# Performance work log

Hardware: AMD Instinct MI355X
Metric: run time of the kernel (lower is better)

The kernel has to match this reference:

```python
import jax, jax.numpy as jnp
import numpy as np

B, N, TOKEN_DIM = 8, 1024, 768
H, D = 12, 64  # n_heads, head_dim


def setup_inputs() -> dict:
    key = jax.random.key(0)
    k1, k2, k3, k4 = jax.random.split(key, 4)
    x = jax.random.normal(k1, (B, N, TOKEN_DIM), dtype=jnp.float32)
    # nn.Linear(token_dim, 3*H*D, bias=False); store as (in, out)
    W_qkv = jax.random.normal(k2, (TOKEN_DIM, 3 * H * D), dtype=jnp.float32) * (TOKEN_DIM ** -0.5)
    # nn.Linear(H*D, token_dim) with bias
    W_out = jax.random.normal(k3, (H * D, TOKEN_DIM), dtype=jnp.float32) * ((H * D) ** -0.5)
    b_out = jax.random.normal(k4, (TOKEN_DIM,), dtype=jnp.float32) * 0.01
    return {"x": x, "W_qkv": W_qkv, "W_out": W_out, "b_out": b_out}


def reference(x, W_qkv, W_out, b_out):
    b, n, _ = x.shape
    qkv = x @ W_qkv                              # (B, N, 3*H*D)
    # Faithful to original: reshape directly to (B, 3, H, N, D)
    qkv = qkv.reshape(b, 3, H, n, D)
    q, k, v = qkv[:, 0], qkv[:, 1], qkv[:, 2]    # each (B, H, N, D)
    scale = D ** -0.5
    scores = jnp.einsum('bhnd,bhmd->bhnm', q, k) * scale
    probs = jax.nn.softmax(scores, axis=-1)
    attn = jnp.einsum('bhnm,bhmd->bhnd', probs, v)  # (B, H, N, D)
    attn = attn.transpose(0, 2, 1, 3).reshape(b, n, H * D)
    out = attn @ W_out + b_out                    # dropout p=0.0 is identity
    return out
```

## Files before the change

kernel.cpp:

```cpp
#include <hip/hip_runtime.h>
#include <math.h>

static constexpr int NB   = 8;
static constexpr int SEQ  = 1024;
static constexpr int TD   = 768;
static constexpr int NH   = 12;
static constexpr int HD   = 64;
static constexpr int QKVC = 3 * NH * HD;

static constexpr size_t BATCH_ELEMS = (size_t)SEQ * QKVC;
static constexpr size_t THIRD_ELEMS = (size_t)NH * SEQ * HD;
static constexpr size_t HEAD_ELEMS  = (size_t)SEQ * HD;

typedef __bf16 bf16x8 __attribute__((ext_vector_type(8)));
typedef __bf16 bf16x4 __attribute__((ext_vector_type(4)));
typedef float  f32x4  __attribute__((ext_vector_type(4)));

#define MFMA16(a, b, c) __builtin_amdgcn_mfma_f32_16x16x32_bf16((a), (b), (c), 0, 0, 0)

static constexpr float SCL2E = 0.18033688011112042f;

__device__ __forceinline__ void gload_lds16(const void* g, void* l) {
  __builtin_amdgcn_global_load_lds(
      (const __attribute__((address_space(1))) unsigned int*)g,
      (__attribute__((address_space(3))) unsigned int*)l, 16, 0, 0);
}

__global__ __launch_bounds__(256) void cast_f32_bf16(const float* __restrict__ in,
                                                     __bf16* __restrict__ out, int n4) {
  int i = blockIdx.x * 256 + threadIdx.x;
  if (i < n4) {
    float4 v = ((const float4*)in)[i];
    bf16x4 o;
    o[0] = (__bf16)v.x; o[1] = (__bf16)v.y; o[2] = (__bf16)v.z; o[3] = (__bf16)v.w;
    ((bf16x4*)out)[i] = o;
  }
}

__global__ __launch_bounds__(256) void wtrans(const float* __restrict__ W,
                                              __bf16* __restrict__ Wt, int K, int N) {
  __shared__ float T[32 * 33];
  const int tid = threadIdx.x;
  const int k0 = blockIdx.y * 32, n0 = blockIdx.x * 32;
#pragma unroll
  for (int i = 0; i < 4; ++i) {
    int idx = tid + i * 256;
    int kk = idx >> 5, nn = idx & 31;
    T[kk * 33 + nn] = W[(size_t)(k0 + kk) * N + n0 + nn];
  }
  __syncthreads();
#pragma unroll
  for (int i = 0; i < 4; ++i) {
    int idx = tid + i * 256;
    int nn = idx >> 5, kk = idx & 31;
    Wt[(size_t)(n0 + nn) * K + k0 + kk] = (__bf16)T[kk * 33 + nn];
  }
}

__global__ __launch_bounds__(256) void vtrans(const __bf16* __restrict__ qkvb,
                                              __bf16* __restrict__ vtb) {
  const int nt = blockIdx.x;
  const int h = blockIdx.y;
  const int b = blockIdx.z;
  __shared__ __bf16 T[128 * 72];
  const int tid = threadIdx.x;
  const int n0 = nt * 128;
  const __bf16* Vb = qkvb + (size_t)b * BATCH_ELEMS + 2 * THIRD_ELEMS + (size_t)h * HEAD_ELEMS;
#pragma unroll
  for (int i = 0; i < 4; ++i) {
    int ch = tid + i * 256;
    int row = ch >> 3, c8 = ch & 7;
    *(bf16x8*)&T[row * 72 + c8 * 8] = *(const bf16x8*)&Vb[(size_t)(n0 + row) * HD + c8 * 8];
  }
  __syncthreads();
#pragma unroll
  for (int i = 0; i < 4; ++i) {
    int ch = tid + i * 256;
    int d = ch >> 4, n8 = ch & 15;
    bf16x8 v;
#pragma unroll
    for (int j = 0; j < 8; ++j) v[j] = T[(n8 * 8 + j) * 72 + d];
    *(bf16x8*)&vtb[((size_t)((b * NH + h) * HD) + d) * SEQ + n0 + n8 * 8] = v;
  }
}

template <int OUT_BF16>
__global__ __launch_bounds__(256) void gemm_mfma(const __bf16* __restrict__ A,
                                                 const __bf16* __restrict__ Bt,
                                                 const float* __restrict__ bias,
                                                 void* __restrict__ C,
                                                 int M, int N, int K) {
  __shared__ __bf16 As[128 * 32];
  __shared__ __bf16 Bs[128 * 32];
  const int tid = threadIdx.x;
  const int lane = tid & 63;
  const int wid = tid >> 6;
  const int wr = wid >> 1, wc = wid & 1;
  const int r = lane & 15, g = lane >> 4;
  const size_t bm = (size_t)blockIdx.y * 128;
  const size_t bn = (size_t)blockIdx.x * 128;

  const int srow = lane >> 2;
  const int scol = (lane & 3) * 8;

  f32x4 acc[4][4];
#pragma unroll
  for (int mi = 0; mi < 4; ++mi)
#pragma unroll
    for (int nj = 0; nj < 4; ++nj) acc[mi][nj] = (f32x4){0.f, 0.f, 0.f, 0.f};

  for (int k0 = 0; k0 < K; k0 += 32) {
#pragma unroll
    for (int j = 0; j < 2; ++j) {
      const int rowbase = wid * 32 + j * 16;
      gload_lds16(&A[(bm + rowbase + srow) * K + k0 + scol], &As[rowbase * 32]);
      gload_lds16(&Bt[(bn + rowbase + srow) * K + k0 + scol], &Bs[rowbase * 32]);
    }
    __syncthreads();
    bf16x8 af[4], bf[4];
#pragma unroll
    for (int mi = 0; mi < 4; ++mi)
      af[mi] = *(const bf16x8*)&As[(wr * 64 + mi * 16 + r) * 32 + g * 8];
#pragma unroll
    for (int nj = 0; nj < 4; ++nj)
      bf[nj] = *(const bf16x8*)&Bs[(wc * 64 + nj * 16 + r) * 32 + g * 8];
#pragma unroll
    for (int mi = 0; mi < 4; ++mi)
#pragma unroll
      for (int nj = 0; nj < 4; ++nj)
        acc[mi][nj] = MFMA16(af[mi], bf[nj], acc[mi][nj]);
    __syncthreads();
  }

  const int orow0 = g * 4;
  const int ocol = r;
#pragma unroll
  for (int mi = 0; mi < 4; ++mi)
#pragma unroll
    for (int nj = 0; nj < 4; ++nj)
#pragma unroll
      for (int reg = 0; reg < 4; ++reg) {
        size_t rrow = bm + wr * 64 + mi * 16 + orow0 + reg;
        size_t ccol = bn + wc * 64 + nj * 16 + ocol;
        float v = acc[mi][nj][reg];
        if (OUT_BF16)
          ((__bf16*)C)[rrow * N + ccol] = (__bf16)v;
        else
          ((float*)C)[rrow * N + ccol] = v + bias[ccol];
      }
}

__global__ __launch_bounds__(256) void attn_mfma(const __bf16* __restrict__ qkvb,
                                                 const __bf16* __restrict__ vtb,
                                                 __bf16* __restrict__ attn2b) {
  const int d = blockIdx.x;
  const int qt = (d >> 3) & 7;
  const int hb = (d >> 6) * 8 + (d & 7);
  const int b = hb / NH, h = hb % NH;

  const int tid = threadIdx.x;
  const int lane = tid & 63;
  const int w = tid >> 6;
  const int c = lane & 15, g = lane >> 4;

  __shared__ __bf16 KsF[2][4096];
  __shared__ __bf16 VsF[2][4096];

  const __bf16* Qb = qkvb + (size_t)b * BATCH_ELEMS + (size_t)h * HEAD_ELEMS;
  const __bf16* Kb = Qb + THIRD_ELEMS;
  const __bf16* Vtb = vtb + (size_t)((b * NH + h) * HD) * SEQ;

  const __bf16* kS[2];
  const __bf16* vS[2];
  int ldsOff[2];
#pragma unroll
  for (int i = 0; i < 2; ++i) {
    const int t2f = i * 4 + w;
    const int t = t2f >> 1, f = t2f & 1;
    const int krow = ((t >> 1) << 5) | ((c >> 2) << 3) | ((t & 1) << 2) | (c & 3);
    kS[i] = Kb + krow * HD + f * 32 + g * 8;
    const int db = t2f >> 1, kk = t2f & 1;
    vS[i] = Vtb + (db * 16 + c) * SEQ + kk * 32 + g * 8;
    ldsOff[i] = t2f * 512;
  }

  bf16x8 qf[2][2];
#pragma unroll
  for (int s = 0; s < 2; ++s) {
    const int q0s = qt * 128 + s * 64 + w * 16;
#pragma unroll
    for (int f = 0; f < 2; ++f)
      qf[s][f] = *(const bf16x8*)&Qb[(size_t)(q0s + c) * HD + f * 32 + g * 8];
  }

  f32x4 Oa[2][4];
#pragma unroll
  for (int s = 0; s < 2; ++s)
#pragma unroll
    for (int db = 0; db < 4; ++db) Oa[s][db] = (f32x4){0.f, 0.f, 0.f, 0.f};
  float lpart[2] = {0.f, 0.f};

#pragma unroll
  for (int i = 0; i < 2; ++i) {
    gload_lds16(kS[i], &KsF[0][ldsOff[i]]);
    gload_lds16(vS[i], &VsF[0][ldsOff[i]]);
    kS[i] += 64 * HD;
    vS[i] += 64;
  }
  __syncthreads();

  int cur = 0;
  for (int it = 0; it < SEQ / 64; ++it) {
    if (it < SEQ / 64 - 1) {
      const int nxt = cur ^ 1;
#pragma unroll
      for (int i = 0; i < 2; ++i) {
        gload_lds16(kS[i], &KsF[nxt][ldsOff[i]]);
        gload_lds16(vS[i], &VsF[nxt][ldsOff[i]]);
        kS[i] += 64 * HD;
        vS[i] += 64;
      }
    }

    f32x4 sa[2][4];
#pragma unroll
    for (int s = 0; s < 2; ++s)
#pragma unroll
      for (int t = 0; t < 4; ++t) sa[s][t] = (f32x4){0.f, 0.f, 0.f, 0.f};
#pragma unroll
    for (int t = 0; t < 4; ++t)
#pragma unroll
      for (int f = 0; f < 2; ++f) {
        bf16x8 kf = *(const bf16x8*)&KsF[cur][(t * 2 + f) * 512 + lane * 8];
        sa[0][t] = MFMA16(kf, qf[0][f], sa[0][t]);
        sa[1][t] = MFMA16(kf, qf[1][f], sa[1][t]);
      }

    bf16x8 pb[2][2];
#pragma unroll
    for (int s = 0; s < 2; ++s) {
      float p[4][4];
      float lp = 0.f;
#pragma unroll
      for (int t = 0; t < 4; ++t)
#pragma unroll
        for (int reg = 0; reg < 4; ++reg) {
          float pv = __builtin_exp2f(sa[s][t][reg] * SCL2E);
          p[t][reg] = pv;
          lp += pv;
        }
      lpart[s] += lp;
#pragma unroll
      for (int kk = 0; kk < 2; ++kk)
#pragma unroll
        for (int i = 0; i < 4; ++i) {
          pb[s][kk][i] = (__bf16)p[2 * kk][i];
          pb[s][kk][4 + i] = (__bf16)p[2 * kk + 1][i];
        }
    }

#pragma unroll
    for (int db = 0; db < 4; ++db)
#pragma unroll
      for (int kk = 0; kk < 2; ++kk) {
        bf16x8 vf = *(const bf16x8*)&VsF[cur][(db * 2 + kk) * 512 + lane * 8];
        Oa[0][db] = MFMA16(vf, pb[0][kk], Oa[0][db]);
        Oa[1][db] = MFMA16(vf, pb[1][kk], Oa[1][db]);
      }

    __syncthreads();
    cur ^= 1;
  }

#pragma unroll
  for (int s = 0; s < 2; ++s) {
    float lrow = lpart[s];
    lrow += __shfl_xor(lrow, 16);
    lrow += __shfl_xor(lrow, 32);
    const float inv = 1.0f / lrow;
    const size_t rowq = (size_t)(b * SEQ) + qt * 128 + s * 64 + w * 16 + c;
#pragma unroll
    for (int db = 0; db < 4; ++db) {
      bf16x4 o;
#pragma unroll
      for (int reg = 0; reg < 4; ++reg) o[reg] = (__bf16)(Oa[s][db][reg] * inv);
      *(bf16x4*)&attn2b[rowq * TD + h * HD + db * 16 + g * 4] = o;
    }
  }
}

extern "C" void kernel_launch(void* const* d_in, const int* in_sizes, int n_in,
                              void* d_out, int out_size, void* d_ws,
                              size_t ws_size, hipStream_t stream) {
  const float* x = (const float*)d_in[0];
  const float* W_qkv = (const float*)d_in[1];
  const float* W_out = (const float*)d_in[2];
  const float* b_out = (const float*)d_in[3];
  float* out = (float*)d_out;

  __bf16* xb = (__bf16*)d_ws;
  __bf16* wqkvt = xb + (size_t)NB * SEQ * TD;
  __bf16* woutt = wqkvt + (size_t)QKVC * TD;
  __bf16* qkvb = woutt + (size_t)TD * TD;
  __bf16* vtb = qkvb + (size_t)NB * SEQ * QKVC;
  __bf16* attn2b = vtb + (size_t)NB * NH * HD * SEQ;

  cast_f32_bf16<<<(NB * SEQ * TD / 4 + 255) / 256, 256, 0, stream>>>(x, xb, NB * SEQ * TD / 4);
  wtrans<<<dim3(QKVC / 32, TD / 32), 256, 0, stream>>>(W_qkv, wqkvt, TD, QKVC);
  wtrans<<<dim3(TD / 32, TD / 32), 256, 0, stream>>>(W_out, woutt, TD, TD);

  gemm_mfma<1><<<dim3(QKVC / 128, NB * SEQ / 128), 256, 0, stream>>>(
      xb, wqkvt, nullptr, qkvb, NB * SEQ, QKVC, TD);

  vtrans<<<dim3(SEQ / 128, NH, NB), 256, 0, stream>>>(qkvb, vtb);

  attn_mfma<<<dim3(SEQ / 128 * NH * NB), 256, 0, stream>>>(qkvb, vtb, attn2b);

  gemm_mfma<0><<<dim3(TD / 128, NB * SEQ / 128), 256, 0, stream>>>(
      attn2b, woutt, b_out, out, NB * SEQ, TD, TD);
}
```

Baseline: 149.4 us.

## Double-buffer GEMM LDS, fold softmax scale into Q, add MFMA priority hints

The GEMM kernel now double-buffers its LDS tiles so the next K-slice load overlaps the current MFMAs. The output projection uses a 64-row tile to launch more blocks. The softmax scale times log2e is applied to Q in the QKV GEMM epilogue, which removes a multiply per score in attention. s_setprio hints wrap the MFMA sections in both the GEMM and attention kernels, and the V-transpose staggers its LDS reads to reduce bank conflicts. Rounding Q to bf16 after scaling slightly changes numerics, and double buffering doubles the GEMM's LDS use.

```diff
diff --git a/kernel.cpp b/kernel.cpp
--- a/kernel.cpp
+++ b/kernel.cpp
@@ -79,74 +79,95 @@
     int d = ch >> 4, n8 = ch & 15;
     bf16x8 v;
 #pragma unroll
-    for (int j = 0; j < 8; ++j) v[j] = T[(n8 * 8 + j) * 72 + d];
+    for (int jj = 0; jj < 8; ++jj) {
+      int j = (jj + n8) & 7;
+      v[j] = T[(n8 * 8 + j) * 72 + d];
+    }
     *(bf16x8*)&vtb[((size_t)((b * NH + h) * HD) + d) * SEQ + n0 + n8 * 8] = v;
   }
 }
 
-template <int OUT_BF16>
+template <int MODE, int BM>
 __global__ __launch_bounds__(256) void gemm_mfma(const __bf16* __restrict__ A,
                                                  const __bf16* __restrict__ Bt,
                                                  const float* __restrict__ bias,
                                                  void* __restrict__ C,
                                                  int M, int N, int K) {
-  __shared__ __bf16 As[128 * 32];
-  __shared__ __bf16 Bs[128 * 32];
+  constexpr int MI = BM / 32;
+  __shared__ __bf16 As[2][BM * 32];
+  __shared__ __bf16 Bs[2][128 * 32];
   const int tid = threadIdx.x;
   const int lane = tid & 63;
   const int wid = tid >> 6;
   const int wr = wid >> 1, wc = wid & 1;
   const int r = lane & 15, g = lane >> 4;
-  const size_t bm = (size_t)blockIdx.y * 128;
+  const size_t bm = (size_t)blockIdx.y * BM;
   const size_t bn = (size_t)blockIdx.x * 128;
 
   const int srow = lane >> 2;
   const int scol = (lane & 3) * 8;
 
-  f32x4 acc[4][4];
-#pragma unroll
-  for (int mi = 0; mi < 4; ++mi)
-#pragma unroll
-    for (int nj = 0; nj < 4; ++nj) acc[mi][nj] = (f32x4){0.f, 0.f, 0.f, 0.f};
-
-  for (int k0 = 0; k0 < K; k0 += 32) {
+  auto stage = [&](int buf, int k0) {
+#pragma unroll
+    for (int j = 0; j < BM / 64; ++j) {
+      const int rowbase = wid * (BM / 4) + j * 16;
+      gload_lds16(&A[(bm + rowbase + srow) * K + k0 + scol], &As[buf][rowbase * 32]);
+    }
 #pragma unroll
     for (int j = 0; j < 2; ++j) {
       const int rowbase = wid * 32 + j * 16;
-      gload_lds16(&A[(bm + rowbase + srow) * K + k0 + scol], &As[rowbase * 32]);
-      gload_lds16(&Bt[(bn + rowbase + srow) * K + k0 + scol], &Bs[rowbase * 32]);
-    }
-    __syncthreads();
-    bf16x8 af[4], bf[4];
-#pragma unroll
-    for (int mi = 0; mi < 4; ++mi)
-      af[mi] = *(const bf16x8*)&As[(wr * 64 + mi * 16 + r) * 32 + g * 8];
+      gload_lds16(&Bt[(bn + rowbase + srow) * K + k0 + scol], &Bs[buf][rowbase * 32]);
+    }
+  };
+
+  f32x4 acc[MI][4];
+#pragma unroll
+  for (int mi = 0; mi < MI; ++mi)
+#pragma unroll
+    for (int nj = 0; nj < 4; ++nj) acc[mi][nj] = (f32x4){0.f, 0.f, 0.f, 0.f};
+
+  stage(0, 0);
+  __syncthreads();
+
+  int cur = 0;
+  for (int k0 = 0; k0 < K; k0 += 32) {
+    if (k0 + 32 < K) stage(cur ^ 1, k0 + 32);
+    bf16x8 af[MI], bf[4];
+#pragma unroll
+    for (int mi = 0; mi < MI; ++mi)
+      af[mi] = *(const bf16x8*)&As[cur][(wr * (BM / 2) + mi * 16 + r) * 32 + g * 8];
 #pragma unroll
     for (int nj = 0; nj < 4; ++nj)
-      bf[nj] = *(const bf16x8*)&Bs[(wc * 64 + nj * 16 + r) * 32 + g * 8];
-#pragma unroll
-    for (int mi = 0; mi < 4; ++mi)
+      bf[nj] = *(const bf16x8*)&Bs[cur][(wc * 64 + nj * 16 + r) * 32 + g * 8];
+    __builtin_amdgcn_s_setprio(1);
+#pragma unroll
+    for (int mi = 0; mi < MI; ++mi)
 #pragma unroll
       for (int nj = 0; nj < 4; ++nj)
         acc[mi][nj] = MFMA16(af[mi], bf[nj], acc[mi][nj]);
+    __builtin_amdgcn_s_setprio(0);
     __syncthreads();
+    cur ^= 1;
   }
 
   const int orow0 = g * 4;
   const int ocol = r;
 #pragma unroll
-  for (int mi = 0; mi < 4; ++mi)
+  for (int mi = 0; mi < MI; ++mi)
 #pragma unroll
     for (int nj = 0; nj < 4; ++nj)
 #pragma unroll
       for (int reg = 0; reg < 4; ++reg) {
-        size_t rrow = bm + wr * 64 + mi * 16 + orow0 + reg;
+        size_t rrow = bm + wr * (BM / 2) + mi * 16 + orow0 + reg;
         size_t ccol = bn + wc * 64 + nj * 16 + ocol;
         float v = acc[mi][nj][reg];
-        if (OUT_BF16)
-          ((__bf16*)C)[rrow * N + ccol] = (__bf16)v;
-        else
+        if (MODE == 1) {
+          int fwb = ((int)(rrow & (SEQ - 1))) * QKVC + (int)ccol;
+          float vv = (fwb < (int)THIRD_ELEMS) ? v * SCL2E : v;
+          ((__bf16*)C)[rrow * N + ccol] = (__bf16)vv;
+        } else {
           ((float*)C)[rrow * N + ccol] = v + bias[ccol];
+        }
       }
 }
 
@@ -227,6 +248,7 @@
     for (int s = 0; s < 2; ++s)
 #pragma unroll
       for (int t = 0; t < 4; ++t) sa[s][t] = (f32x4){0.f, 0.f, 0.f, 0.f};
+    __builtin_amdgcn_s_setprio(1);
 #pragma unroll
     for (int t = 0; t < 4; ++t)
 #pragma unroll
@@ -235,6 +257,7 @@
         sa[0][t] = MFMA16(kf, qf[0][f], sa[0][t]);
         sa[1][t] = MFMA16(kf, qf[1][f], sa[1][t]);
       }
+    __builtin_amdgcn_s_setprio(0);
 
     bf16x8 pb[2][2];
 #pragma unroll
@@ -245,7 +268,7 @@
       for (int t = 0; t < 4; ++t)
 #pragma unroll
         for (int reg = 0; reg < 4; ++reg) {
-          float pv = __builtin_exp2f(sa[s][t][reg] * SCL2E);
+          float pv = __builtin_exp2f(sa[s][t][reg]);
           p[t][reg] = pv;
           lp += pv;
         }
@@ -259,6 +282,7 @@
         }
     }
 
+    __builtin_amdgcn_s_setprio(1);
 #pragma unroll
     for (int db = 0; db < 4; ++db)
 #pragma unroll
@@ -267,6 +291,7 @@
         Oa[0][db] = MFMA16(vf, pb[0][kk], Oa[0][db]);
         Oa[1][db] = MFMA16(vf, pb[1][kk], Oa[1][db]);
       }
+    __builtin_amdgcn_s_setprio(0);
 
     __syncthreads();
     cur ^= 1;
@@ -309,13 +334,13 @@
   wtrans<<<dim3(QKVC / 32, TD / 32), 256, 0, stream>>>(W_qkv, wqkvt, TD, QKVC);
   wtrans<<<dim3(TD / 32, TD / 32), 256, 0, stream>>>(W_out, woutt, TD, TD);
 
-  gemm_mfma<1><<<dim3(QKVC / 128, NB * SEQ / 128), 256, 0, stream>>>(
+  gemm_mfma<1, 128><<<dim3(QKVC / 128, NB * SEQ / 128), 256, 0, stream>>>(
       xb, wqkvt, nullptr, qkvb, NB * SEQ, QKVC, TD);
 
   vtrans<<<dim3(SEQ / 128, NH, NB), 256, 0, stream>>>(qkvb, vtb);
 
   attn_mfma<<<dim3(SEQ / 128 * NH * NB), 256, 0, stream>>>(qkvb, vtb, attn2b);
 
-  gemm_mfma<0><<<dim3(TD / 128, NB * SEQ / 128), 256, 0, stream>>>(
+  gemm_mfma<0, 64><<<dim3(TD / 128, NB * SEQ / 64), 256, 0, stream>>>(
       attn2b, woutt, b_out, out, NB * SEQ, TD, TD);
 }
```

After: 153.3 us. 2.6% more time.
